# Kernel optimization log

Hardware: AMD Instinct MI355X
Metric: run time of the kernel (lower is better)

## Reference

```python
import jax, jax.numpy as jnp
import numpy as np

LRELU = 0.01
EPS = 1e-5
HEADS = 4


def _ln(x, g, b):
    m = x.mean(-1, keepdims=True)
    v = ((x - m) ** 2).mean(-1, keepdims=True)
    return (x - m) / jnp.sqrt(v + EPS) * g + b


def _mapx(x, w1, b1, g1, be1, w2, b2, g2, be2, w3, b3):
    h = jax.nn.leaky_relu(_ln(x @ w1 + b1, g1, be1), LRELU)
    h = jax.nn.leaky_relu(_ln(h @ w2 + b2, g2, be2), LRELU)
    return h @ w3 + b3


def _mcab(x, y, wq, bq, wk, bk, wv, bv, wo, bo, rescale):
    # spectral (channel-wise) multi-head cross attention: q from x, k/v from y
    b, c, h, w = x.shape
    n = h * w
    xt = x.reshape(b, c, n).transpose(0, 2, 1)  # (b, n, c)
    yt = y.reshape(b, c, n).transpose(0, 2, 1)
    dh = c // HEADS
    q = (xt @ wq + bq).reshape(b, n, HEADS, dh).transpose(0, 2, 3, 1)  # (b,H,dh,n)
    k = (yt @ wk + bk).reshape(b, n, HEADS, dh).transpose(0, 2, 3, 1)
    v = (yt @ wv + bv).reshape(b, n, HEADS, dh).transpose(0, 2, 3, 1)
    q = q / (jnp.linalg.norm(q, axis=-1, keepdims=True) + 1e-8)
    k = k / (jnp.linalg.norm(k, axis=-1, keepdims=True) + 1e-8)
    attn = jax.nn.softmax(jnp.einsum('bhdn,bhen->bhde', q, k) * rescale, axis=-1)  # (b,H,dh,dh)
    out = jnp.einsum('bhde,bhen->bhdn', attn, v)  # (b,H,dh,n)
    out = out.transpose(0, 3, 1, 2).reshape(b, n, c) @ wo + bo
    out = out + xt  # residual
    return out.transpose(0, 2, 1).reshape(b, c, h, w)


def setup_inputs() -> dict:
    key = jax.random.key(0)
    ks = jax.random.split(key, 16)
    B, C, H, W, K = 4, 64, 128, 128, 21
    s = 0.02
    nrm = lambda k, shape: jax.random.normal(k, shape, jnp.float32) * s
    return {
        'x': jax.random.normal(ks[0], (B, C, H, W), jnp.float32),
        'semantic': jax.random.uniform(ks[1], (B, K, H, W), jnp.float32),
        'wa': nrm(ks[2], (1, C, 4)), 'ba': jnp.zeros((1, 4), jnp.float32),
        'wb': nrm(ks[3], (20, C, 3)), 'bb': jnp.zeros((20, 3), jnp.float32),
        'in_w': nrm(ks[4], (C, C)), 'in_b': jnp.zeros((C,), jnp.float32),
        'mx_w1': nrm(ks[5], (C, 2 * C)), 'mx_b1': jnp.zeros((2 * C,), jnp.float32),
        'mx_g1': jnp.ones((2 * C,), jnp.float32), 'mx_be1': jnp.zeros((2 * C,), jnp.float32),
        'mx_w2': nrm(ks[6], (2 * C, 2 * C)), 'mx_b2': jnp.zeros((2 * C,), jnp.float32),
        'mx_g2': jnp.ones((2 * C,), jnp.float32), 'mx_be2': jnp.zeros((2 * C,), jnp.float32),
        'mx_w3': nrm(ks[7], (2 * C, C)), 'mx_b3': jnp.zeros((C,), jnp.float32),
        'wq': nrm(ks[8], (C, C)), 'bq': jnp.zeros((C,), jnp.float32),
        'wk': nrm(ks[9], (C, C)), 'bk': jnp.zeros((C,), jnp.float32),
        'wv': nrm(ks[10], (C, C)), 'bv': jnp.zeros((C,), jnp.float32),
        'wo': nrm(ks[11], (C, C)), 'bo': jnp.zeros((C,), jnp.float32),
        'rescale': jnp.ones((HEADS, 1, 1), jnp.float32),
    }


def reference(x, semantic, wa, ba, wb, bb, in_w, in_b,
              mx_w1, mx_b1, mx_g1, mx_be1, mx_w2, mx_b2, mx_g2, mx_be2,
              mx_w3, mx_b3, wq, bq, wk, bk, wv, bv, wo, bo, rescale):
    sem = jax.nn.relu(semantic)            # (b,K,h,w)
    xh = x.transpose(0, 2, 3, 1)           # (b,h,w,c)
    # per-class mask-multiply: (b,K,h,w,c)
    masked = xh[:, None] * sem[:, :, :, :, None]
    # class 0 gets the extra channel (64 = 1*4 + 20*3)
    feat_a = jnp.einsum('bkhwc,kcd->bkhwd', masked[:, :1], wa) + ba[None, :, None, None, :]
    feat_b = jnp.einsum('bkhwc,kcd->bkhwd', masked[:, 1:], wb) + bb[None, :, None, None, :]
    b, _, h, w, _ = feat_a.shape
    feat_a = feat_a.reshape(b, h, w, 4)
    feat_b = jnp.moveaxis(feat_b, 1, 3).reshape(b, h, w, 60)  # preserve class order
    all_feat = jnp.concatenate([feat_a, feat_b], axis=-1)     # (b,h,w,64)
    y = (all_feat @ in_w + in_b).transpose(0, 3, 1, 2)        # (b,c,h,w)
    xm = _mapx(xh, mx_w1, mx_b1, mx_g1, mx_be1, mx_w2, mx_b2, mx_g2, mx_be2, mx_w3, mx_b3)
    xm = xm.transpose(0, 3, 1, 2)
    return _mcab(xm, y, wq, bq, wk, bk, wv, bv, wo, bo, rescale)
```

## Files before the change

kernel.cpp:

```cpp
#include <hip/hip_runtime.h>
#include <hip/hip_bf16.h>

#define NPX 16384
using bf16 = __hip_bfloat16;
typedef __attribute__((ext_vector_type(8))) short short8;
typedef __attribute__((ext_vector_type(4))) short short4v;
typedef __attribute__((ext_vector_type(4))) float f32x4;

#define DEV static __device__ __forceinline__

DEV float lrelu(float v) { return v >= 0.f ? v : 0.01f * v; }
DEV short f2b(float f) { __hip_bfloat16 h = __float2bfloat16(f); return *reinterpret_cast<short*>(&h); }
DEV float b2f(short s) { __hip_bfloat16 h; *reinterpret_cast<short*>(&h) = s; return __bfloat162float(h); }
DEV f32x4 mfma16(short8 a, short8 b, f32x4 c) {
    return __builtin_amdgcn_mfma_f32_16x16x32_bf16(a, b, c, 0, 0, 0);
}

template<int K, int NT>
DEV void gemm(const short* __restrict__ A, int px0, int pitch,
              const short* __restrict__ WT, f32x4 acc[2][NT])
{
    int lane = threadIdx.x & 63;
    int ln = lane & 15, q8 = (lane >> 4) * 8;
    const short* a0p = A + (size_t)(px0 + ln) * pitch + q8;
    const short* a1p = a0p + 16 * pitch;
    const short* bp  = WT + ln * K + q8;
#pragma unroll
    for (int c0 = 0; c0 < K; c0 += 32) {
        short8 a0 = *(const short8*)(a0p + c0);
        short8 a1 = *(const short8*)(a1p + c0);
#pragma unroll
        for (int t = 0; t < NT; ++t) {
            short8 b = *(const short8*)(bp + (size_t)t * 16 * K + c0);
            acc[0][t] = mfma16(a0, b, acc[0][t]);
            acc[1][t] = mfma16(a1, b, acc[1][t]);
        }
    }
}

template<int NT>
DEV void acc_bias(f32x4 acc[2][NT], const float* __restrict__ bias)
{
    int ln = threadIdx.x & 15;
#pragma unroll
    for (int t = 0; t < NT; ++t) {
        float bv = bias[t * 16 + ln];
        f32x4 v = {bv, bv, bv, bv};
        acc[0][t] = v; acc[1][t] = v;
    }
}

template<int NT>
DEV void acc_zero(f32x4 acc[2][NT])
{
    f32x4 z = {0.f, 0.f, 0.f, 0.f};
#pragma unroll
    for (int t = 0; t < NT; ++t) { acc[0][t] = z; acc[1][t] = z; }
}

template<int NT, int PITCH>
DEV void dstore(f32x4 acc[2][NT], short* sD, int px0)
{
    int lane = threadIdx.x & 63;
    int ln = lane & 15, r0 = (lane >> 4) * 4;
#pragma unroll
    for (int m = 0; m < 2; ++m)
#pragma unroll
        for (int t = 0; t < NT; ++t)
#pragma unroll
            for (int r = 0; r < 4; ++r)
                sD[(px0 + m * 16 + r0 + r) * PITCH + t * 16 + ln] = f2b(acc[m][t][r]);
}

template<int CW, int PITCH>
DEV void copyout(const short* sD, short* __restrict__ dst)
{
    int tid = threadIdx.x;
#pragma unroll
    for (int j = 0; j < (128 * CW) / 2048; ++j) {
        int idx = j * 2048 + tid * 8;
        int px = idx / CW, c = idx % CW;
        short8 v = *(const short8*)(&sD[px * PITCH + c]);
        *reinterpret_cast<short8*>(dst + (size_t)px * CW + c) = v;
    }
}

DEV void stage_x64(const float* __restrict__ xb, int nbase, short* sA)
{
    int tid = threadIdx.x;
#pragma unroll
    for (int it = 0; it < 8; ++it) {
        int item = it * 256 + tid;
        int n = item & 127, cg = item >> 7;
        float v0 = xb[(cg * 4 + 0) * NPX + nbase + n];
        float v1 = xb[(cg * 4 + 1) * NPX + nbase + n];
        float v2 = xb[(cg * 4 + 2) * NPX + nbase + n];
        float v3 = xb[(cg * 4 + 3) * NPX + nbase + n];
        short4v pk = {f2b(v0), f2b(v1), f2b(v2), f2b(v3)};
        *reinterpret_cast<short4v*>(&sA[n * 72 + cg * 4]) = pk;
    }
}

__global__ __launch_bounds__(256) void k_prep(const float* __restrict__ wa,
                                              const float* __restrict__ wb,
                                              const float* __restrict__ in_w,
                                              const float* __restrict__ w1,
                                              const float* __restrict__ w2,
                                              const float* __restrict__ w3,
                                              const float* __restrict__ wq,
                                              const float* __restrict__ wk,
                                              const float* __restrict__ wv,
                                              short* __restrict__ wt)
{
    int idx = blockIdx.x * 256 + threadIdx.x;
    float v;
    if (idx < 4096) {
        int j = idx >> 6, c = idx & 63;
        v = (j < 4) ? wa[c * 4 + j] : wb[((j - 4) / 3) * 192 + c * 3 + ((j - 4) % 3)];
    } else if (idx < 8192) {
        int i = idx - 4096; int e = i >> 6, k = i & 63; v = in_w[k * 64 + e];
    } else if (idx < 16384) {
        int i = idx - 8192; int e = i >> 6, k = i & 63; v = w1[k * 128 + e];
    } else if (idx < 32768) {
        int i = idx - 16384; int e = i >> 7, k = i & 127; v = w2[k * 128 + e];
    } else if (idx < 40960) {
        int i = idx - 32768; int e = i >> 7, k = i & 127; v = w3[k * 64 + e];
    } else if (idx < 45056) {
        int i = idx - 40960; int e = i >> 6, k = i & 63; v = wq[k * 64 + e];
    } else {
        int i = idx - 45056; int e = i >> 6, k = i & 63;
        v = (e < 64) ? wk[k * 64 + e] : wv[k * 64 + (e - 64)];
    }
    wt[idx] = f2b(v);
}

__global__ __launch_bounds__(256) void k_fyk(const float* __restrict__ x,
                                             const float* __restrict__ sem,
                                             const float* __restrict__ ba,
                                             const float* __restrict__ bbv,
                                             const float* __restrict__ in_b,
                                             const float* __restrict__ bk,
                                             const float* __restrict__ bv,
                                             const short* __restrict__ wt,
                                             short* __restrict__ kvout)
{
    __shared__ short sA[128 * 136];
    int tid = threadIdx.x, w = tid >> 6, lane = tid & 63;
    int ln = lane & 15, qd = lane >> 4;
    int pxb = blockIdx.x * 128;
    int b = pxb >> 14, nbase = pxb & (NPX - 1);
    const float* xb = x + (size_t)b * 64 * NPX;
    int px0 = w * 32;

    stage_x64(xb, nbase, sA);
    __syncthreads();

    f32x4 a1[2][4];
    acc_zero<4>(a1);
    gemm<64, 4>(sA, px0, 72, wt + 0, a1);
    __syncthreads();
#pragma unroll
    for (int m = 0; m < 2; ++m)
#pragma unroll
        for (int t = 0; t < 4; ++t) {
            int j = t * 16 + ln;
            int cls = (j < 4) ? 0 : 1 + (j - 4) / 3;
            float bias = (j < 4) ? ba[j] : bbv[j - 4];
            int rg = nbase + px0 + m * 16 + qd * 4;
            f32x4 sm4 = *(const f32x4*)(sem + ((size_t)b * 21 + cls) * NPX + rg);
#pragma unroll
            for (int r = 0; r < 4; ++r)
                sA[(px0 + m * 16 + qd * 4 + r) * 72 + j] =
                    f2b(fmaxf(sm4[r], 0.f) * a1[m][t][r] + bias);
        }
    __syncthreads();

    f32x4 a2[2][4];
    acc_bias<4>(a2, in_b);
    gemm<64, 4>(sA, px0, 72, wt + 4096, a2);
    __syncthreads();
    dstore<4, 72>(a2, sA, px0);
    __syncthreads();

    f32x4 a3[2][8];
    {
        int lnn = tid & 15;
#pragma unroll
        for (int t = 0; t < 8; ++t) {
            float bvv = (t < 4) ? bk[t * 16 + lnn] : bv[(t - 4) * 16 + lnn];
            f32x4 vv = {bvv, bvv, bvv, bvv};
            a3[0][t] = vv; a3[1][t] = vv;
        }
    }
    gemm<64, 8>(sA, px0, 72, wt + 45056, a3);
    __syncthreads();
    dstore<8, 136>(a3, sA, px0);
    __syncthreads();
    copyout<128, 136>(sA, kvout + (size_t)pxb * 128);
}

DEV void ln_pass(short* sD, float* s_mean, float* s_rs,
                 const float* __restrict__ g, const float* __restrict__ be,
                 short* __restrict__ gout)
{
    int tid = threadIdx.x;
    int px = tid >> 1, half = (tid & 1) * 64;
    float s = 0.f, ss = 0.f;
#pragma unroll
    for (int j = 0; j < 8; ++j) {
        short8 v8 = *(const short8*)(&sD[px * 136 + half + j * 8]);
#pragma unroll
        for (int e = 0; e < 8; ++e) { float f = b2f(v8[e]); s += f; ss += f * f; }
    }
    s += __shfl_xor(s, 1); ss += __shfl_xor(ss, 1);
    if ((tid & 1) == 0) {
        float m = s * (1.f / 128.f);
        float var = ss * (1.f / 128.f) - m * m;
        s_mean[px] = m; s_rs[px] = rsqrtf(var + 1e-5f);
    }
    __syncthreads();
#pragma unroll
    for (int j = 0; j < 8; ++j) {
        int idx = j * 2048 + tid * 8;
        int p2 = idx >> 7, c = idx & 127;
        short8 v8 = *(const short8*)(&sD[p2 * 136 + c]);
        float m = s_mean[p2], r = s_rs[p2];
        f32x4 g0 = *(const f32x4*)(g + c), g1v = *(const f32x4*)(g + c + 4);
        f32x4 b0 = *(const f32x4*)(be + c), b1v = *(const f32x4*)(be + c + 4);
        short8 o;
#pragma unroll
        for (int e = 0; e < 8; ++e) {
            float gg = (e < 4) ? g0[e] : g1v[e - 4];
            float bb = (e < 4) ? b0[e] : b1v[e - 4];
            o[e] = f2b(lrelu((b2f(v8[e]) - m) * r * gg + bb));
        }
        if (gout) *reinterpret_cast<short8*>(gout + (size_t)idx) = o;
        else      *reinterpret_cast<short8*>(&sD[p2 * 136 + c]) = o;
    }
}

__global__ __launch_bounds__(256) void k_m12(const float* __restrict__ x,
                                             const float* __restrict__ b1,
                                             const float* __restrict__ g1,
                                             const float* __restrict__ be1,
                                             const float* __restrict__ b2,
                                             const float* __restrict__ g2,
                                             const float* __restrict__ be2,
                                             const short* __restrict__ wt,
                                             short* __restrict__ h2out)
{
    __shared__ short sA[128 * 136];
    __shared__ float s_mean[128], s_rs[128];
    int tid = threadIdx.x, w = tid >> 6;
    int pxb = blockIdx.x * 128;
    int b = pxb >> 14, nbase = pxb & (NPX - 1);
    const float* xb = x + (size_t)b * 64 * NPX;
    int px0 = w * 32;

    stage_x64(xb, nbase, sA);
    __syncthreads();

    f32x4 acc[2][8];
    acc_bias<8>(acc, b1);
    gemm<64, 8>(sA, px0, 72, wt + 8192, acc);
    __syncthreads();
    dstore<8, 136>(acc, sA, px0);
    __syncthreads();
    ln_pass(sA, s_mean, s_rs, g1, be1, nullptr);
    __syncthreads();

    acc_bias<8>(acc, b2);
    gemm<128, 8>(sA, px0, 136, wt + 16384, acc);
    __syncthreads();
    dstore<8, 136>(acc, sA, px0);
    __syncthreads();
    ln_pass(sA, s_mean, s_rs, g2, be2, h2out + (size_t)pxb * 128);
}

__global__ __launch_bounds__(256) void k_m3q(const short* __restrict__ h2,
                                             const float* __restrict__ b3,
                                             const float* __restrict__ bq,
                                             const short* __restrict__ wt,
                                             short* __restrict__ xm,
                                             short* __restrict__ q)
{
    __shared__ short sA[128 * 72];
    int tid = threadIdx.x, w = tid >> 6;
    int pxb = blockIdx.x * 128;
    int px0 = w * 32;

    f32x4 acc[2][4];
    acc_bias<4>(acc, b3);
    gemm<128, 4>(h2 + (size_t)pxb * 128, px0, 128, wt + 32768, acc);
    dstore<4, 72>(acc, sA, px0);
    __syncthreads();
    copyout<64, 72>(sA, xm + (size_t)pxb * 64);

    f32x4 a2[2][4];
    acc_bias<4>(a2, bq);
    gemm<64, 4>(sA, px0, 72, wt + 40960, a2);
    __syncthreads();
    dstore<4, 72>(a2, sA, px0);
    __syncthreads();
    copyout<64, 72>(sA, q + (size_t)pxb * 64);
}

__global__ __launch_bounds__(256) void k_gram(const short* __restrict__ q,
                                              const short* __restrict__ kv,
                                              float* __restrict__ gram,
                                              float* __restrict__ nsq)
{
    __shared__ short sQ[4][16 * 264];
    __shared__ short sK[4][16 * 264];
    int tid = threadIdx.x, w = tid >> 6, lane = tid & 63;
    int ln = lane & 15, q8 = (lane >> 4) * 8, qd = lane >> 4;
    int bh = blockIdx.x >> 4;
    int b = bh >> 2, h = bh & 3;
    int nb = (blockIdx.x & 15) * 1024 + w * 256;
    size_t pxg = (size_t)b * NPX + nb;

#pragma unroll
    for (int it = 0; it < 8; ++it) {
        int item = it * 64 + lane;
        int px = item & 255, dc = item >> 8;
        short8 qv = *(const short8*)(q + (pxg + px) * 64 + h * 16 + dc * 8);
        short8 kvv = *(const short8*)(kv + (pxg + px) * 128 + h * 16 + dc * 8);
#pragma unroll
        for (int jj = 0; jj < 8; ++jj) {
            sQ[w][(dc * 8 + jj) * 264 + px] = qv[jj];
            sK[w][(dc * 8 + jj) * 264 + px] = kvv[jj];
        }
    }
    __syncthreads();

    f32x4 aqk = {0,0,0,0}, aqq = {0,0,0,0}, akk = {0,0,0,0};
#pragma unroll
    for (int s = 0; s < 8; ++s) {
        short8 a = *(const short8*)(&sQ[w][ln * 264 + s * 32 + q8]);
        short8 bf = *(const short8*)(&sK[w][ln * 264 + s * 32 + q8]);
        aqk = mfma16(a, bf, aqk);
        aqq = mfma16(a, a, aqq);
        akk = mfma16(bf, bf, akk);
    }
    int e = ln;
#pragma unroll
    for (int r = 0; r < 4; ++r) {
        int d = qd * 4 + r;
        atomicAdd(&gram[bh * 256 + d * 16 + e], aqk[r]);
        if (e == d) {
            atomicAdd(&nsq[bh * 16 + d], aqq[r]);
            atomicAdd(&nsq[256 + bh * 16 + d], akk[r]);
        }
    }
}

__global__ __launch_bounds__(256) void k_attnM(const float* __restrict__ gram,
                                               const float* __restrict__ nsq,
                                               const float* __restrict__ rescale,
                                               const float* __restrict__ wo,
                                               short* __restrict__ MT)
{
    __shared__ float s_at[1024];
    int b = blockIdx.x, tid = threadIdx.x;
    if (tid < 64) {
        int h = tid >> 4, d = tid & 15;
        float nq = sqrtf(nsq[b * 64 + h * 16 + d]) + 1e-8f;
        float rsc = rescale[h];
        float lg[16];
#pragma unroll
        for (int e = 0; e < 16; ++e) {
            float nk = sqrtf(nsq[256 + b * 64 + h * 16 + e]) + 1e-8f;
            lg[e] = rsc * gram[b * 1024 + h * 256 + d * 16 + e] / (nq * nk);
        }
        float m = lg[0];
#pragma unroll
        for (int e = 1; e < 16; ++e) m = fmaxf(m, lg[e]);
        float ssum = 0.f;
#pragma unroll
        for (int e = 0; e < 16; ++e) { lg[e] = expf(lg[e] - m); ssum += lg[e]; }
        float inv = 1.f / ssum;
#pragma unroll
        for (int e = 0; e < 16; ++e) s_at[h * 256 + d * 16 + e] = lg[e] * inv;
    }
    __syncthreads();
    int he = tid >> 2, h = he >> 4, e = he & 15;
    int cc0 = (tid & 3) * 16;
#pragma unroll
    for (int cx = 0; cx < 16; ++cx) {
        int cc = cc0 + cx;
        float s = 0.f;
#pragma unroll
        for (int d = 0; d < 16; ++d)
            s = fmaf(s_at[h * 256 + d * 16 + e], wo[(h * 16 + d) * 64 + cc], s);
        MT[b * 4096 + cc * 64 + he] = f2b(s);
    }
}

__global__ __launch_bounds__(256) void k_out(const short* __restrict__ kv,
                                             const short* __restrict__ xm,
                                             const short* __restrict__ MT,
                                             const float* __restrict__ bo,
                                             float* __restrict__ out)
{
    int tid = threadIdx.x, w = tid >> 6, lane = tid & 63;
    int ln = lane & 15, qd = lane >> 4;
    int pxb = blockIdx.x * 128;
    int b = pxb >> 14, nbase = pxb & (NPX - 1);
    int px0 = w * 32;

    f32x4 acc[2][4];
    acc_bias<4>(acc, bo);
    gemm<64, 4>(kv + (size_t)pxb * 128 + 64, px0, 128, MT + b * 4096, acc);

#pragma unroll
    for (int m = 0; m < 2; ++m)
#pragma unroll
        for (int t = 0; t < 4; ++t) {
            int c = t * 16 + ln;
            int n = nbase + px0 + m * 16 + qd * 4;
            const short* xp = xm + ((size_t)pxb + px0 + m * 16 + qd * 4) * 64 + c;
            f32x4 v;
#pragma unroll
            for (int r = 0; r < 4; ++r) v[r] = acc[m][t][r] + b2f(xp[r * 64]);
            *reinterpret_cast<f32x4*>(out + ((size_t)b * 64 + c) * NPX + n) = v;
        }
}

extern "C" void kernel_launch(void* const* d_in, const int* in_sizes, int n_in,
                              void* d_out, int out_size, void* d_ws, size_t ws_size,
                              hipStream_t stream)
{
    const float* x    = (const float*)d_in[0];
    const float* sem  = (const float*)d_in[1];
    const float* wa   = (const float*)d_in[2];
    const float* ba   = (const float*)d_in[3];
    const float* wb   = (const float*)d_in[4];
    const float* bbv  = (const float*)d_in[5];
    const float* in_w = (const float*)d_in[6];
    const float* in_b = (const float*)d_in[7];
    const float* w1   = (const float*)d_in[8];
    const float* b1   = (const float*)d_in[9];
    const float* g1   = (const float*)d_in[10];
    const float* be1  = (const float*)d_in[11];
    const float* w2   = (const float*)d_in[12];
    const float* b2   = (const float*)d_in[13];
    const float* g2   = (const float*)d_in[14];
    const float* be2  = (const float*)d_in[15];
    const float* w3   = (const float*)d_in[16];
    const float* b3   = (const float*)d_in[17];
    const float* wq   = (const float*)d_in[18];
    const float* bq   = (const float*)d_in[19];
    const float* wk   = (const float*)d_in[20];
    const float* bk   = (const float*)d_in[21];
    const float* wv   = (const float*)d_in[22];
    const float* bv   = (const float*)d_in[23];
    const float* wo   = (const float*)d_in[24];
    const float* bo   = (const float*)d_in[25];
    const float* rescale = (const float*)d_in[26];

    char* wsb = (char*)d_ws;
    short* wt   = (short*)wsb;
    short* kv   = (short*)(wsb + (1 << 20));
    short* h2   = (short*)(wsb + (1 << 20) + (16u << 20));
    short* xmp  = (short*)(wsb + (1 << 20) + (32u << 20));
    short* qp   = (short*)(wsb + (1 << 20) + (40u << 20));
    float* gram = (float*)(wsb + (1 << 20) + (48u << 20));
    float* nsq  = gram + 4096;
    short* MT   = (short*)(nsq + 512);

    dim3 blk(256);
    k_prep<<<dim3(208), blk, 0, stream>>>(wa, wb, in_w, w1, w2, w3, wq, wk, wv, wt);
    hipMemsetAsync(gram, 0, (4096 + 512) * sizeof(float), stream);
    k_fyk<<<dim3(512), blk, 0, stream>>>(x, sem, ba, bbv, in_b, bk, bv, wt, kv);
    k_m12<<<dim3(512), blk, 0, stream>>>(x, b1, g1, be1, b2, g2, be2, wt, h2);
    k_m3q<<<dim3(512), blk, 0, stream>>>(h2, b3, bq, wt, xmp, qp);
    k_gram<<<dim3(256), blk, 0, stream>>>(qp, kv, gram, nsq);
    k_attnM<<<dim3(4), blk, 0, stream>>>(gram, nsq, rescale, wo, MT);
    k_out<<<dim3(512), blk, 0, stream>>>(kv, xmp, MT, bo, (float*)d_out);
}
```

Baseline: 194.1 us.

## Fuse MLP stages into one per-wave kernel with split-bf16 GEMMs

Merges the two MLP kernels into a single kernel that keeps each wave's 16-pixel tile in registers and wave-private shared memory. The kernel does layer norm in registers via shuffles, so block-wide barriers and the h2 round trip through global memory go away. It also adds hi/lo bf16 splitting (three MFMA passes per GEMM) to recover fp32-like accuracy in the MLP, stores xm in fp32, and splits k/v into separate arrays with smaller tiles and doubled grids. The extra MFMA work and doubled weight table trade compute for precision and lower memory traffic.

```diff
diff --git a/kernel.cpp b/kernel.cpp
--- a/kernel.cpp
+++ b/kernel.cpp
@@ -4,10 +4,21 @@
 #define NPX 16384
 using bf16 = __hip_bfloat16;
 typedef __attribute__((ext_vector_type(8))) short short8;
-typedef __attribute__((ext_vector_type(4))) short short4v;
 typedef __attribute__((ext_vector_type(4))) float f32x4;
 
 #define DEV static __device__ __forceinline__
+
+#define WAB   0
+#define WINW  4096
+#define W1HI  8192
+#define W1LO  16384
+#define W2HI  24576
+#define W2LO  40960
+#define W3HI  57344
+#define W3LO  65536
+#define WQT   73728
+#define WKV   77824
+#define WTOT  86016
 
 DEV float lrelu(float v) { return v >= 0.f ? v : 0.01f * v; }
 DEV short f2b(float f) { __hip_bfloat16 h = __float2bfloat16(f); return *reinterpret_cast<short*>(&h); }
@@ -17,89 +28,140 @@
 }
 
 template<int K, int NT>
-DEV void gemm(const short* __restrict__ A, int px0, int pitch,
-              const short* __restrict__ WT, f32x4 acc[2][NT])
+DEV void gemm1(const short* __restrict__ A, int pitch,
+               const short* __restrict__ WT, f32x4* acc)
 {
     int lane = threadIdx.x & 63;
     int ln = lane & 15, q8 = (lane >> 4) * 8;
-    const short* a0p = A + (size_t)(px0 + ln) * pitch + q8;
-    const short* a1p = a0p + 16 * pitch;
-    const short* bp  = WT + ln * K + q8;
+    const short* ap = A + (size_t)ln * pitch + q8;
+    const short* bp = WT + ln * K + q8;
 #pragma unroll
     for (int c0 = 0; c0 < K; c0 += 32) {
-        short8 a0 = *(const short8*)(a0p + c0);
-        short8 a1 = *(const short8*)(a1p + c0);
+        short8 a = *(const short8*)(ap + c0);
 #pragma unroll
         for (int t = 0; t < NT; ++t) {
             short8 b = *(const short8*)(bp + (size_t)t * 16 * K + c0);
-            acc[0][t] = mfma16(a0, b, acc[0][t]);
-            acc[1][t] = mfma16(a1, b, acc[1][t]);
+            acc[t] = mfma16(a, b, acc[t]);
         }
     }
 }
 
 template<int NT>
-DEV void acc_bias(f32x4 acc[2][NT], const float* __restrict__ bias)
+DEV void acc_bias1(f32x4* acc, const float* __restrict__ bias)
 {
     int ln = threadIdx.x & 15;
 #pragma unroll
     for (int t = 0; t < NT; ++t) {
         float bv = bias[t * 16 + ln];
         f32x4 v = {bv, bv, bv, bv};
-        acc[0][t] = v; acc[1][t] = v;
+        acc[t] = v;
     }
 }
 
 template<int NT>
-DEV void acc_zero(f32x4 acc[2][NT])
-{
-    f32x4 z = {0.f, 0.f, 0.f, 0.f};
-#pragma unroll
-    for (int t = 0; t < NT; ++t) { acc[0][t] = z; acc[1][t] = z; }
-}
-
-template<int NT, int PITCH>
-DEV void dstore(f32x4 acc[2][NT], short* sD, int px0)
+DEV void dstore1(const f32x4* acc, short* sD, int pitch)
 {
     int lane = threadIdx.x & 63;
     int ln = lane & 15, r0 = (lane >> 4) * 4;
 #pragma unroll
-    for (int m = 0; m < 2; ++m)
-#pragma unroll
-        for (int t = 0; t < NT; ++t)
-#pragma unroll
-            for (int r = 0; r < 4; ++r)
-                sD[(px0 + m * 16 + r0 + r) * PITCH + t * 16 + ln] = f2b(acc[m][t][r]);
-}
-
-template<int CW, int PITCH>
-DEV void copyout(const short* sD, short* __restrict__ dst)
-{
-    int tid = threadIdx.x;
-#pragma unroll
-    for (int j = 0; j < (128 * CW) / 2048; ++j) {
-        int idx = j * 2048 + tid * 8;
-        int px = idx / CW, c = idx % CW;
-        short8 v = *(const short8*)(&sD[px * PITCH + c]);
-        *reinterpret_cast<short8*>(dst + (size_t)px * CW + c) = v;
-    }
-}
-
-DEV void stage_x64(const float* __restrict__ xb, int nbase, short* sA)
-{
-    int tid = threadIdx.x;
-#pragma unroll
-    for (int it = 0; it < 8; ++it) {
-        int item = it * 256 + tid;
-        int n = item & 127, cg = item >> 7;
-        float v0 = xb[(cg * 4 + 0) * NPX + nbase + n];
-        float v1 = xb[(cg * 4 + 1) * NPX + nbase + n];
-        float v2 = xb[(cg * 4 + 2) * NPX + nbase + n];
-        float v3 = xb[(cg * 4 + 3) * NPX + nbase + n];
-        short4v pk = {f2b(v0), f2b(v1), f2b(v2), f2b(v3)};
-        *reinterpret_cast<short4v*>(&sA[n * 72 + cg * 4]) = pk;
-    }
-}
+    for (int t = 0; t < NT; ++t)
+#pragma unroll
+        for (int r = 0; r < 4; ++r)
+            sD[(r0 + r) * pitch + t * 16 + ln] = f2b(acc[t][r]);
+}
+
+template<int NT>
+DEV void split_store(const f32x4* acc, short* hi, short* lo, int pitch)
+{
+    int lane = threadIdx.x & 63;
+    int ln = lane & 15, r0 = (lane >> 4) * 4;
+#pragma unroll
+    for (int t = 0; t < NT; ++t)
+#pragma unroll
+        for (int r = 0; r < 4; ++r) {
+            float v = acc[t][r];
+            short h = f2b(v);
+            hi[(r0 + r) * pitch + t * 16 + ln] = h;
+            lo[(r0 + r) * pitch + t * 16 + ln] = f2b(v - b2f(h));
+        }
+}
+
+template<int NT>
+DEV void ln_reg(f32x4* acc, const float* __restrict__ g, const float* __restrict__ be)
+{
+    int lane = threadIdx.x & 63, ln = lane & 15;
+    f32x4 s = {0,0,0,0}, ss = {0,0,0,0};
+#pragma unroll
+    for (int t = 0; t < NT; ++t)
+#pragma unroll
+        for (int r = 0; r < 4; ++r) { float v = acc[t][r]; s[r] += v; ss[r] += v * v; }
+#pragma unroll
+    for (int off = 1; off < 16; off <<= 1)
+#pragma unroll
+        for (int r = 0; r < 4; ++r) {
+            s[r] += __shfl_xor(s[r], off);
+            ss[r] += __shfl_xor(ss[r], off);
+        }
+    f32x4 mm, rs;
+#pragma unroll
+    for (int r = 0; r < 4; ++r) {
+        float m = s[r] * (1.f / 128.f);
+        float var = ss[r] * (1.f / 128.f) - m * m;
+        mm[r] = m; rs[r] = rsqrtf(var + 1e-5f);
+    }
+#pragma unroll
+    for (int t = 0; t < NT; ++t) {
+        float gg = g[t * 16 + ln], bb = be[t * 16 + ln];
+#pragma unroll
+        for (int r = 0; r < 4; ++r)
+            acc[t][r] = lrelu((acc[t][r] - mm[r]) * rs[r] * gg + bb);
+    }
+}
+
+DEV void copyout16(const short* sD, int pitch, short* __restrict__ dst)
+{
+    int lane = threadIdx.x & 63;
+    int px = lane >> 2, c = (lane & 3) * 16;
+    short8 v0 = *(const short8*)(&sD[px * pitch + c]);
+    short8 v1 = *(const short8*)(&sD[px * pitch + c + 8]);
+    *reinterpret_cast<short8*>(dst + (size_t)px * 64 + c) = v0;
+    *reinterpret_cast<short8*>(dst + (size_t)px * 64 + c + 8) = v1;
+}
+
+DEV void stage_x16(const float* __restrict__ xb, int n0, short* X)
+{
+    int lane = threadIdx.x & 63;
+    int ln = lane & 15, qd = lane >> 4;
+    float vb[16];
+#pragma unroll
+    for (int t = 0; t < 16; ++t) vb[t] = xb[(size_t)(qd * 16 + t) * NPX + n0 + ln];
+    short8 lo, hi;
+#pragma unroll
+    for (int t = 0; t < 8; ++t) { lo[t] = f2b(vb[t]); hi[t] = f2b(vb[8 + t]); }
+    *reinterpret_cast<short8*>(&X[ln * 72 + qd * 16]) = lo;
+    *reinterpret_cast<short8*>(&X[ln * 72 + qd * 16 + 8]) = hi;
+}
+
+DEV void stage_x16_split(const float* __restrict__ xb, int n0, short* Xhi, short* Xlo)
+{
+    int lane = threadIdx.x & 63;
+    int ln = lane & 15, qd = lane >> 4;
+    float vb[16];
+#pragma unroll
+    for (int t = 0; t < 16; ++t) vb[t] = xb[(size_t)(qd * 16 + t) * NPX + n0 + ln];
+    short8 h0, h1, l0, l1;
+#pragma unroll
+    for (int t = 0; t < 8; ++t) {
+        float v = vb[t];     short h = f2b(v); h0[t] = h; l0[t] = f2b(v - b2f(h));
+        float v2 = vb[8 + t]; short h2 = f2b(v2); h1[t] = h2; l1[t] = f2b(v2 - b2f(h2));
+    }
+    *reinterpret_cast<short8*>(&Xhi[ln * 72 + qd * 16]) = h0;
+    *reinterpret_cast<short8*>(&Xhi[ln * 72 + qd * 16 + 8]) = h1;
+    *reinterpret_cast<short8*>(&Xlo[ln * 72 + qd * 16]) = l0;
+    *reinterpret_cast<short8*>(&Xlo[ln * 72 + qd * 16 + 8]) = l1;
+}
+
+DEV float wlo(float w) { return w - b2f(f2b(w)); }
 
 __global__ __launch_bounds__(256) void k_prep(const float* __restrict__ wa,
                                               const float* __restrict__ wb,
@@ -113,22 +175,29 @@
                                               short* __restrict__ wt)
 {
     int idx = blockIdx.x * 256 + threadIdx.x;
+    if (idx >= WTOT) return;
     float v;
-    if (idx < 4096) {
+    if (idx < WINW) {
         int j = idx >> 6, c = idx & 63;
         v = (j < 4) ? wa[c * 4 + j] : wb[((j - 4) / 3) * 192 + c * 3 + ((j - 4) % 3)];
-    } else if (idx < 8192) {
-        int i = idx - 4096; int e = i >> 6, k = i & 63; v = in_w[k * 64 + e];
-    } else if (idx < 16384) {
-        int i = idx - 8192; int e = i >> 6, k = i & 63; v = w1[k * 128 + e];
-    } else if (idx < 32768) {
-        int i = idx - 16384; int e = i >> 7, k = i & 127; v = w2[k * 128 + e];
-    } else if (idx < 40960) {
-        int i = idx - 32768; int e = i >> 7, k = i & 127; v = w3[k * 64 + e];
-    } else if (idx < 45056) {
-        int i = idx - 40960; int e = i >> 6, k = i & 63; v = wq[k * 64 + e];
+    } else if (idx < W1HI) {
+        int i = idx - WINW; v = in_w[(i & 63) * 64 + (i >> 6)];
+    } else if (idx < W1LO) {
+        int i = idx - W1HI; v = w1[(i & 63) * 128 + (i >> 6)];
+    } else if (idx < W2HI) {
+        int i = idx - W1LO; v = wlo(w1[(i & 63) * 128 + (i >> 6)]);
+    } else if (idx < W2LO) {
+        int i = idx - W2HI; v = w2[(i & 127) * 128 + (i >> 7)];
+    } else if (idx < W3HI) {
+        int i = idx - W2LO; v = wlo(w2[(i & 127) * 128 + (i >> 7)]);
+    } else if (idx < W3LO) {
+        int i = idx - W3HI; v = w3[(i & 127) * 64 + (i >> 7)];
+    } else if (idx < WQT) {
+        int i = idx - W3LO; v = wlo(w3[(i & 127) * 64 + (i >> 7)]);
+    } else if (idx < WKV) {
+        int i = idx - WQT; v = wq[(i & 63) * 64 + (i >> 6)];
     } else {
-        int i = idx - 45056; int e = i >> 6, k = i & 63;
+        int i = idx - WKV; int e = i >> 6, k = i & 63;
         v = (e < 64) ? wk[k * 64 + e] : wv[k * 64 + (e - 64)];
     }
     wt[idx] = f2b(v);
@@ -142,205 +211,156 @@
                                              const float* __restrict__ bk,
                                              const float* __restrict__ bv,
                                              const short* __restrict__ wt,
-                                             short* __restrict__ kvout)
-{
-    __shared__ short sA[128 * 136];
+                                             short* __restrict__ kout,
+                                             short* __restrict__ vout)
+{
+    __shared__ short smem[4][3][16 * 72];
     int tid = threadIdx.x, w = tid >> 6, lane = tid & 63;
     int ln = lane & 15, qd = lane >> 4;
-    int pxb = blockIdx.x * 128;
-    int b = pxb >> 14, nbase = pxb & (NPX - 1);
+    int pw = blockIdx.x * 64 + w * 16;
+    int b = pw >> 14, n0 = pw & (NPX - 1);
     const float* xb = x + (size_t)b * 64 * NPX;
-    int px0 = w * 32;
-
-    stage_x64(xb, nbase, sA);
-    __syncthreads();
-
-    f32x4 a1[2][4];
-    acc_zero<4>(a1);
-    gemm<64, 4>(sA, px0, 72, wt + 0, a1);
-    __syncthreads();
-#pragma unroll
-    for (int m = 0; m < 2; ++m)
-#pragma unroll
-        for (int t = 0; t < 4; ++t) {
-            int j = t * 16 + ln;
-            int cls = (j < 4) ? 0 : 1 + (j - 4) / 3;
-            float bias = (j < 4) ? ba[j] : bbv[j - 4];
-            int rg = nbase + px0 + m * 16 + qd * 4;
-            f32x4 sm4 = *(const f32x4*)(sem + ((size_t)b * 21 + cls) * NPX + rg);
-#pragma unroll
-            for (int r = 0; r < 4; ++r)
-                sA[(px0 + m * 16 + qd * 4 + r) * 72 + j] =
-                    f2b(fmaxf(sm4[r], 0.f) * a1[m][t][r] + bias);
-        }
-    __syncthreads();
-
-    f32x4 a2[2][4];
-    acc_bias<4>(a2, in_b);
-    gemm<64, 4>(sA, px0, 72, wt + 4096, a2);
-    __syncthreads();
-    dstore<4, 72>(a2, sA, px0);
-    __syncthreads();
-
-    f32x4 a3[2][8];
-    {
-        int lnn = tid & 15;
-#pragma unroll
-        for (int t = 0; t < 8; ++t) {
-            float bvv = (t < 4) ? bk[t * 16 + lnn] : bv[(t - 4) * 16 + lnn];
-            f32x4 vv = {bvv, bvv, bvv, bvv};
-            a3[0][t] = vv; a3[1][t] = vv;
-        }
-    }
-    gemm<64, 8>(sA, px0, 72, wt + 45056, a3);
-    __syncthreads();
-    dstore<8, 136>(a3, sA, px0);
-    __syncthreads();
-    copyout<128, 136>(sA, kvout + (size_t)pxb * 128);
-}
-
-DEV void ln_pass(short* sD, float* s_mean, float* s_rs,
-                 const float* __restrict__ g, const float* __restrict__ be,
-                 short* __restrict__ gout)
-{
-    int tid = threadIdx.x;
-    int px = tid >> 1, half = (tid & 1) * 64;
-    float s = 0.f, ss = 0.f;
-#pragma unroll
-    for (int j = 0; j < 8; ++j) {
-        short8 v8 = *(const short8*)(&sD[px * 136 + half + j * 8]);
-#pragma unroll
-        for (int e = 0; e < 8; ++e) { float f = b2f(v8[e]); s += f; ss += f * f; }
-    }
-    s += __shfl_xor(s, 1); ss += __shfl_xor(ss, 1);
-    if ((tid & 1) == 0) {
-        float m = s * (1.f / 128.f);
-        float var = ss * (1.f / 128.f) - m * m;
-        s_mean[px] = m; s_rs[px] = rsqrtf(var + 1e-5f);
-    }
-    __syncthreads();
-#pragma unroll
-    for (int j = 0; j < 8; ++j) {
-        int idx = j * 2048 + tid * 8;
-        int p2 = idx >> 7, c = idx & 127;
-        short8 v8 = *(const short8*)(&sD[p2 * 136 + c]);
-        float m = s_mean[p2], r = s_rs[p2];
-        f32x4 g0 = *(const f32x4*)(g + c), g1v = *(const f32x4*)(g + c + 4);
-        f32x4 b0 = *(const f32x4*)(be + c), b1v = *(const f32x4*)(be + c + 4);
-        short8 o;
-#pragma unroll
-        for (int e = 0; e < 8; ++e) {
-            float gg = (e < 4) ? g0[e] : g1v[e - 4];
-            float bb = (e < 4) ? b0[e] : b1v[e - 4];
-            o[e] = f2b(lrelu((b2f(v8[e]) - m) * r * gg + bb));
-        }
-        if (gout) *reinterpret_cast<short8*>(gout + (size_t)idx) = o;
-        else      *reinterpret_cast<short8*>(&sD[p2 * 136 + c]) = o;
-    }
-}
-
-__global__ __launch_bounds__(256) void k_m12(const float* __restrict__ x,
+    short* X  = smem[w][0];
+    short* S1 = smem[w][1];
+    short* S2 = smem[w][2];
+
+    stage_x16(xb, n0, X);
+
+    f32x4 a1[4];
+    { f32x4 z = {0,0,0,0}; for (int t = 0; t < 4; ++t) a1[t] = z; }
+    gemm1<64, 4>(X, 72, wt + WAB, a1);
+#pragma unroll
+    for (int t = 0; t < 4; ++t) {
+        int j = t * 16 + ln;
+        int cls = (j < 4) ? 0 : 1 + (j - 4) / 3;
+        float bias = (j < 4) ? ba[j] : bbv[j - 4];
+        f32x4 sm4 = *(const f32x4*)(sem + ((size_t)b * 21 + cls) * NPX + n0 + qd * 4);
+#pragma unroll
+        for (int r = 0; r < 4; ++r)
+            S1[(qd * 4 + r) * 72 + j] = f2b(fmaxf(sm4[r], 0.f) * a1[t][r] + bias);
+    }
+
+    f32x4 a2[4];
+    acc_bias1<4>(a2, in_b);
+    gemm1<64, 4>(S1, 72, wt + WINW, a2);
+    dstore1<4>(a2, S2, 72);
+
+    f32x4 a3[8];
+    acc_bias1<4>(a3, bk);
+    acc_bias1<4>(a3 + 4, bv);
+    gemm1<64, 8>(S2, 72, wt + WKV, a3);
+    dstore1<4>(a3, S1, 72);
+    dstore1<4>(a3 + 4, X, 72);
+    copyout16(S1, 72, kout + (size_t)pw * 64);
+    copyout16(X, 72, vout + (size_t)pw * 64);
+}
+
+__global__ __launch_bounds__(256) void k_mlp(const float* __restrict__ x,
                                              const float* __restrict__ b1,
                                              const float* __restrict__ g1,
                                              const float* __restrict__ be1,
                                              const float* __restrict__ b2,
                                              const float* __restrict__ g2,
                                              const float* __restrict__ be2,
-                                             const short* __restrict__ wt,
-                                             short* __restrict__ h2out)
-{
-    __shared__ short sA[128 * 136];
-    __shared__ float s_mean[128], s_rs[128];
-    int tid = threadIdx.x, w = tid >> 6;
-    int pxb = blockIdx.x * 128;
-    int b = pxb >> 14, nbase = pxb & (NPX - 1);
-    const float* xb = x + (size_t)b * 64 * NPX;
-    int px0 = w * 32;
-
-    stage_x64(xb, nbase, sA);
-    __syncthreads();
-
-    f32x4 acc[2][8];
-    acc_bias<8>(acc, b1);
-    gemm<64, 8>(sA, px0, 72, wt + 8192, acc);
-    __syncthreads();
-    dstore<8, 136>(acc, sA, px0);
-    __syncthreads();
-    ln_pass(sA, s_mean, s_rs, g1, be1, nullptr);
-    __syncthreads();
-
-    acc_bias<8>(acc, b2);
-    gemm<128, 8>(sA, px0, 136, wt + 16384, acc);
-    __syncthreads();
-    dstore<8, 136>(acc, sA, px0);
-    __syncthreads();
-    ln_pass(sA, s_mean, s_rs, g2, be2, h2out + (size_t)pxb * 128);
-}
-
-__global__ __launch_bounds__(256) void k_m3q(const short* __restrict__ h2,
                                              const float* __restrict__ b3,
                                              const float* __restrict__ bq,
                                              const short* __restrict__ wt,
-                                             short* __restrict__ xm,
-                                             short* __restrict__ q)
-{
-    __shared__ short sA[128 * 72];
-    int tid = threadIdx.x, w = tid >> 6;
-    int pxb = blockIdx.x * 128;
-    int px0 = w * 32;
-
-    f32x4 acc[2][4];
-    acc_bias<4>(acc, b3);
-    gemm<128, 4>(h2 + (size_t)pxb * 128, px0, 128, wt + 32768, acc);
-    dstore<4, 72>(acc, sA, px0);
-    __syncthreads();
-    copyout<64, 72>(sA, xm + (size_t)pxb * 64);
-
-    f32x4 a2[2][4];
-    acc_bias<4>(a2, bq);
-    gemm<64, 4>(sA, px0, 72, wt + 40960, a2);
-    __syncthreads();
-    dstore<4, 72>(a2, sA, px0);
-    __syncthreads();
-    copyout<64, 72>(sA, q + (size_t)pxb * 64);
+                                             float* __restrict__ xmout,
+                                             short* __restrict__ qout)
+{
+    __shared__ short sX[4][2 * 16 * 72];
+    __shared__ short sH[4][16 * 136];
+    __shared__ short sL[4][16 * 136];
+    int tid = threadIdx.x, w = tid >> 6, lane = tid & 63;
+    int ln = lane & 15, qd = lane >> 4, r0 = qd * 4;
+    int pw = blockIdx.x * 64 + w * 16;
+    int b = pw >> 14, n0 = pw & (NPX - 1);
+    const float* xb = x + (size_t)b * 64 * NPX;
+    short* Xhi = sX[w];
+    short* Xlo = sX[w] + 16 * 72;
+    short* S1h = sH[w];
+    short* S1l = sL[w];
+
+    stage_x16_split(xb, n0, Xhi, Xlo);
+
+    f32x4 acc[8];
+    acc_bias1<8>(acc, b1);
+    gemm1<64, 8>(Xhi, 72, wt + W1HI, acc);
+    gemm1<64, 8>(Xhi, 72, wt + W1LO, acc);
+    gemm1<64, 8>(Xlo, 72, wt + W1HI, acc);
+    ln_reg<8>(acc, g1, be1);
+    split_store<8>(acc, S1h, S1l, 136);
+
+    acc_bias1<8>(acc, b2);
+    gemm1<128, 8>(S1h, 136, wt + W2HI, acc);
+    gemm1<128, 8>(S1h, 136, wt + W2LO, acc);
+    gemm1<128, 8>(S1l, 136, wt + W2HI, acc);
+    ln_reg<8>(acc, g2, be2);
+    split_store<8>(acc, S1h, S1l, 136);
+
+    f32x4 a3[4];
+    acc_bias1<4>(a3, b3);
+    gemm1<128, 4>(S1h, 136, wt + W3HI, a3);
+    gemm1<128, 4>(S1h, 136, wt + W3LO, a3);
+    gemm1<128, 4>(S1l, 136, wt + W3HI, a3);
+
+    float* XF = (float*)sX[w];
+#pragma unroll
+    for (int t = 0; t < 4; ++t)
+#pragma unroll
+        for (int r = 0; r < 4; ++r)
+            XF[(r0 + r) * 68 + t * 16 + ln] = a3[t][r];
+    {
+        int px = lane >> 2, c = (lane & 3) * 16;
+#pragma unroll
+        for (int j = 0; j < 4; ++j) {
+            f32x4 vv = *(const f32x4*)(&XF[px * 68 + c + j * 4]);
+            *reinterpret_cast<f32x4*>(xmout + (size_t)(pw + px) * 64 + c + j * 4) = vv;
+        }
+    }
+
+    dstore1<4>(a3, S1h, 136);
+    f32x4 aq[4];
+    acc_bias1<4>(aq, bq);
+    gemm1<64, 4>(S1h, 136, wt + WQT, aq);
+    dstore1<4>(aq, S1l, 136);
+    copyout16(S1l, 136, qout + (size_t)pw * 64);
 }
 
 __global__ __launch_bounds__(256) void k_gram(const short* __restrict__ q,
-                                              const short* __restrict__ kv,
+                                              const short* __restrict__ k,
                                               float* __restrict__ gram,
                                               float* __restrict__ nsq)
 {
-    __shared__ short sQ[4][16 * 264];
-    __shared__ short sK[4][16 * 264];
+    __shared__ short sQ[4][16 * 136], sK[4][16 * 136];
     int tid = threadIdx.x, w = tid >> 6, lane = tid & 63;
     int ln = lane & 15, q8 = (lane >> 4) * 8, qd = lane >> 4;
-    int bh = blockIdx.x >> 4;
+    int bh = blockIdx.x >> 5;
     int b = bh >> 2, h = bh & 3;
-    int nb = (blockIdx.x & 15) * 1024 + w * 256;
+    int nb = (blockIdx.x & 31) * 512 + w * 128;
     size_t pxg = (size_t)b * NPX + nb;
 
 #pragma unroll
-    for (int it = 0; it < 8; ++it) {
-        int item = it * 64 + lane;
-        int px = item & 255, dc = item >> 8;
-        short8 qv = *(const short8*)(q + (pxg + px) * 64 + h * 16 + dc * 8);
-        short8 kvv = *(const short8*)(kv + (pxg + px) * 128 + h * 16 + dc * 8);
-#pragma unroll
-        for (int jj = 0; jj < 8; ++jj) {
-            sQ[w][(dc * 8 + jj) * 264 + px] = qv[jj];
-            sK[w][(dc * 8 + jj) * 264 + px] = kvv[jj];
-        }
-    }
-    __syncthreads();
+    for (int it = 0; it < 4; ++it) {
+        int idx = it * 64 + lane;
+        int px = idx >> 1, half = idx & 1;
+        short8 qv = *(const short8*)(q + (pxg + px) * 64 + h * 16 + half * 8);
+        short8 kv = *(const short8*)(k + (pxg + px) * 64 + h * 16 + half * 8);
+#pragma unroll
+        for (int j = 0; j < 8; ++j) {
+            sQ[w][(half * 8 + j) * 136 + px] = qv[j];
+            sK[w][(half * 8 + j) * 136 + px] = kv[j];
+        }
+    }
 
     f32x4 aqk = {0,0,0,0}, aqq = {0,0,0,0}, akk = {0,0,0,0};
 #pragma unroll
-    for (int s = 0; s < 8; ++s) {
-        short8 a = *(const short8*)(&sQ[w][ln * 264 + s * 32 + q8]);
-        short8 bf = *(const short8*)(&sK[w][ln * 264 + s * 32 + q8]);
-        aqk = mfma16(a, bf, aqk);
+    for (int s = 0; s < 4; ++s) {
+        short8 a  = *(const short8*)(&sQ[w][ln * 136 + s * 32 + q8]);
+        short8 bb = *(const short8*)(&sK[w][ln * 136 + s * 32 + q8]);
+        aqk = mfma16(a, bb, aqk);
         aqq = mfma16(a, a, aqq);
-        akk = mfma16(bf, bf, akk);
+        akk = mfma16(bb, bb, akk);
     }
     int e = ln;
 #pragma unroll
@@ -396,34 +416,30 @@
     }
 }
 
-__global__ __launch_bounds__(256) void k_out(const short* __restrict__ kv,
-                                             const short* __restrict__ xm,
+__global__ __launch_bounds__(256) void k_out(const short* __restrict__ v,
+                                             const float* __restrict__ xmf,
                                              const short* __restrict__ MT,
                                              const float* __restrict__ bo,
                                              float* __restrict__ out)
 {
     int tid = threadIdx.x, w = tid >> 6, lane = tid & 63;
     int ln = lane & 15, qd = lane >> 4;
-    int pxb = blockIdx.x * 128;
-    int b = pxb >> 14, nbase = pxb & (NPX - 1);
-    int px0 = w * 32;
-
-    f32x4 acc[2][4];
-    acc_bias<4>(acc, bo);
-    gemm<64, 4>(kv + (size_t)pxb * 128 + 64, px0, 128, MT + b * 4096, acc);
-
-#pragma unroll
-    for (int m = 0; m < 2; ++m)
-#pragma unroll
-        for (int t = 0; t < 4; ++t) {
-            int c = t * 16 + ln;
-            int n = nbase + px0 + m * 16 + qd * 4;
-            const short* xp = xm + ((size_t)pxb + px0 + m * 16 + qd * 4) * 64 + c;
-            f32x4 v;
-#pragma unroll
-            for (int r = 0; r < 4; ++r) v[r] = acc[m][t][r] + b2f(xp[r * 64]);
-            *reinterpret_cast<f32x4*>(out + ((size_t)b * 64 + c) * NPX + n) = v;
-        }
+    int pw = blockIdx.x * 64 + w * 16;
+    int b = pw >> 14, n0 = pw & (NPX - 1);
+
+    f32x4 acc[4];
+    acc_bias1<4>(acc, bo);
+    gemm1<64, 4>(v + (size_t)pw * 64, 64, MT + b * 4096, acc);
+
+#pragma unroll
+    for (int t = 0; t < 4; ++t) {
+        int c = t * 16 + ln;
+        f32x4 o;
+#pragma unroll
+        for (int r = 0; r < 4; ++r)
+            o[r] = acc[t][r] + xmf[(size_t)(pw + qd * 4 + r) * 64 + c];
+        *reinterpret_cast<f32x4*>(out + ((size_t)b * 64 + c) * NPX + n0 + qd * 4) = o;
+    }
 }
 
 extern "C" void kernel_launch(void* const* d_in, const int* in_sizes, int n_in,
@@ -460,21 +476,20 @@
 
     char* wsb = (char*)d_ws;
     short* wt   = (short*)wsb;
-    short* kv   = (short*)(wsb + (1 << 20));
-    short* h2   = (short*)(wsb + (1 << 20) + (16u << 20));
-    short* xmp  = (short*)(wsb + (1 << 20) + (32u << 20));
-    short* qp   = (short*)(wsb + (1 << 20) + (40u << 20));
-    float* gram = (float*)(wsb + (1 << 20) + (48u << 20));
+    short* kpx  = (short*)(wsb + (1u << 20));
+    short* vpx  = (short*)(wsb + (1u << 20) + (8u << 20));
+    float* xmf  = (float*)(wsb + (1u << 20) + (16u << 20));
+    short* qpx  = (short*)(wsb + (1u << 20) + (32u << 20));
+    float* gram = (float*)(wsb + (1u << 20) + (40u << 20));
     float* nsq  = gram + 4096;
     short* MT   = (short*)(nsq + 512);
 
     dim3 blk(256);
-    k_prep<<<dim3(208), blk, 0, stream>>>(wa, wb, in_w, w1, w2, w3, wq, wk, wv, wt);
+    k_prep<<<dim3(336), blk, 0, stream>>>(wa, wb, in_w, w1, w2, w3, wq, wk, wv, wt);
     hipMemsetAsync(gram, 0, (4096 + 512) * sizeof(float), stream);
-    k_fyk<<<dim3(512), blk, 0, stream>>>(x, sem, ba, bbv, in_b, bk, bv, wt, kv);
-    k_m12<<<dim3(512), blk, 0, stream>>>(x, b1, g1, be1, b2, g2, be2, wt, h2);
-    k_m3q<<<dim3(512), blk, 0, stream>>>(h2, b3, bq, wt, xmp, qp);
-    k_gram<<<dim3(256), blk, 0, stream>>>(qp, kv, gram, nsq);
+    k_fyk<<<dim3(1024), blk, 0, stream>>>(x, sem, ba, bbv, in_b, bk, bv, wt, kpx, vpx);
+    k_mlp<<<dim3(1024), blk, 0, stream>>>(x, b1, g1, be1, b2, g2, be2, b3, bq, wt, xmf, qpx);
+    k_gram<<<dim3(512), blk, 0, stream>>>(qpx, kpx, gram, nsq);
     k_attnM<<<dim3(4), blk, 0, stream>>>(gram, nsq, rescale, wo, MT);
-    k_out<<<dim3(512), blk, 0, stream>>>(kv, xmp, MT, bo, (float*)d_out);
-}
+    k_out<<<dim3(1024), blk, 0, stream>>>(vpx, xmf, MT, bo, (float*)d_out);
+}
```

After: 252.8 us. 30.2% more time.
